# Kernel optimization log

Hardware: AMD Instinct MI355X
Metric: run time of the kernel (lower is better)

Reference implementation:

```python
import jax, jax.numpy as jnp
import numpy as np

B, L, D, H = 8192, 32, 128, 8  # batch nodes, max neighbors, embed dim, heads


def setup_inputs() -> dict:
    key = jax.random.key(0)
    ks = jax.random.split(key, 16)
    s = 0.05  # weight init scale
    return {
        "node_embeds": jax.random.normal(ks[0], (B, D), jnp.float32),
        "neighbor_embeds": jax.random.normal(ks[1], (B, L, D), jnp.float32),
        "node_degrees": jax.random.randint(ks[2], (B,), 1, L + 1),
        # layer 0 (concatenate=True): query_heads 128->1024, value_proj 128->128
        "wq0": jax.random.normal(ks[3], (H * D, D), jnp.float32) * s,
        "bq0": jax.random.normal(ks[4], (H * D,), jnp.float32) * s,
        "wv0": jax.random.normal(ks[5], (D, D), jnp.float32) * s,
        "bv0": jax.random.normal(ks[6], (D,), jnp.float32) * s,
        "wp0": jax.random.normal(ks[7], (D, D), jnp.float32) * s,
        "bp0": jax.random.normal(ks[8], (D,), jnp.float32) * s,
        # layer 1 (last, concatenate=False): query_heads 128->1024, value_proj 128->1024
        "wq1": jax.random.normal(ks[9], (H * D, D), jnp.float32) * s,
        "bq1": jax.random.normal(ks[10], (H * D,), jnp.float32) * s,
        "wv1": jax.random.normal(ks[11], (H * D, D), jnp.float32) * s,
        "bv1": jax.random.normal(ks[12], (H * D,), jnp.float32) * s,
        "wp1": jax.random.normal(ks[13], (D, D), jnp.float32) * s,
        "bp1": jax.random.normal(ks[14], (D,), jnp.float32) * s,
    }


def _attn_layer(node, neigh, mask, wq, bq, wv, bv, wp, bp, concatenate):
    # neigh: [B, L, D] (already zero-masked); mask: [B, L] bool
    b, l, d = neigh.shape
    dk = d  # attnhead_size == query_size == D for use_dot=True
    v = neigh @ wv.T + bv                      # [B, L, H*dv]
    dv = v.shape[-1] // H
    v = v.reshape(b, l, H, dv).transpose(0, 2, 1, 3)   # [B, H, L, dv]
    q = (node @ wq.T + bq).reshape(b, H, dk)           # [B, H, dk]
    scores = jnp.einsum('bhd,bld->bhl', q, neigh) / jnp.sqrt(jnp.float32(dk))
    scores = jnp.where(mask[:, None, :], scores, jnp.float32(-1e9))
    p = jax.nn.softmax(scores, axis=-1)                # [B, H, L]
    av = jnp.einsum('bhl,bhld->bhd', p, v)             # [B, H, dv]
    av = av.reshape(b, H * dv) if concatenate else av.mean(axis=1)
    return node @ wp.T + bp + av


def reference(node_embeds, neighbor_embeds, node_degrees,
              wq0, bq0, wv0, bv0, wp0, bp0,
              wq1, bq1, wv1, bv1, wp1, bp1):
    mask = jnp.arange(L)[None, :] < node_degrees[:, None]          # [B, L]
    neigh = jnp.where(mask[:, :, None], neighbor_embeds, 0.0)
    x = _attn_layer(node_embeds, neigh, mask, wq0, bq0, wv0, bv0, wp0, bp0, True)
    x = jax.nn.relu(x)  # activation on all but last layer
    x = _attn_layer(x, neigh, mask, wq1, bq1, wv1, bv1, wp1, bp1, False)
    return x
```

## Files before the change

kernel.cpp:

```cpp
#include <hip/hip_runtime.h>

constexpr int Ln = 32, Dn = 128, Hn = 8;

using bf16x8 = __attribute__((ext_vector_type(8))) short;
using f32x4  = __attribute__((ext_vector_type(4))) float;

__device__ __forceinline__ unsigned short f2bf(float f) {
    union { float f; unsigned u; } v; v.f = f;
    unsigned r = v.u + 0x7FFFu + ((v.u >> 16) & 1u);
    return (unsigned short)(r >> 16);
}
__device__ __forceinline__ float bf2f(unsigned short s) {
    union { unsigned u; float f; } v; v.u = ((unsigned)s) << 16; return v.f;
}
__device__ __forceinline__ bf16x8 cvt8(float4 a, float4 b) {
    bf16x8 r;
    r[0] = (short)f2bf(a.x); r[1] = (short)f2bf(a.y);
    r[2] = (short)f2bf(a.z); r[3] = (short)f2bf(a.w);
    r[4] = (short)f2bf(b.x); r[5] = (short)f2bf(b.y);
    r[6] = (short)f2bf(b.z); r[7] = (short)f2bf(b.w);
    return r;
}

constexpr int    CVT_ITEMS = 442368 + 2304;
constexpr size_t WS_NEED   = 442368ull * 2 + 2304ull * 4;

__global__ void cvt_weights(const float* __restrict__ wq0, const float* __restrict__ bq0,
                            const float* __restrict__ wv0, const float* __restrict__ bv0,
                            const float* __restrict__ wp0, const float* __restrict__ bp0,
                            const float* __restrict__ wq1, const float* __restrict__ bq1,
                            const float* __restrict__ wv1, const float* __restrict__ bv1,
                            const float* __restrict__ wp1, const float* __restrict__ bp1,
                            unsigned short* __restrict__ ws)
{
    const float scale = 0.08838834764831845f;
    int tid = blockIdx.x * 256 + threadIdx.x;
    if (tid >= CVT_ITEMS) return;
    if (tid < 442368) {
        float v;
        if      (tid < 131072) v = wq0[tid] * scale;
        else if (tid < 262144) v = wq1[tid - 131072] * scale;
        else if (tid < 278528) v = wv0[tid - 262144];
        else if (tid < 294912) v = wp0[tid - 278528];
        else if (tid < 425984) v = wv1[tid - 294912] * 0.125f;
        else                   v = wp1[tid - 425984];
        ws[tid] = f2bf(v);
    } else {
        int j = tid - 442368;
        float* fws = (float*)(ws + 442368);
        if      (j < 1024) fws[j] = bq0[j] * scale;
        else if (j < 2048) fws[j] = bq1[j - 1024] * scale;
        else if (j < 2176) { int d = j - 2048; fws[j] = bp0[d] + bv0[d]; }
        else if (j < 2304) {
            int d = j - 2176;
            float s = 0.f;
            #pragma unroll
            for (int h = 0; h < Hn; ++h) s += bv1[h * Dn + d];
            fws[j] = bp1[d] + 0.125f * s;
        }
    }
}

__global__ __launch_bounds__(512, 4)
void gcn15(const float* __restrict__ nodeE, const float* __restrict__ neighE,
           const int* __restrict__ degp, const unsigned short* __restrict__ ws,
           float* __restrict__ out)
{
    __shared__ unsigned short sN[8][16][136];
    __shared__ unsigned short sQC[16 * 1096];
    __shared__ unsigned short sX[16][136];
    __shared__ float          sP[8][16][Hn];
    __shared__ float          sSum[8][Hn];
    __shared__ int            sDeg[16];

    const unsigned short* wq0b = ws;
    const unsigned short* wq1b = ws + 131072;
    const unsigned short* wv0b = ws + 262144;
    const unsigned short* wp0b = ws + 278528;
    const unsigned short* wv1b = ws + 294912;
    const unsigned short* wp1b = ws + 425984;
    const float* fws  = (const float*)(ws + 442368);
    const float* bq0s = fws;
    const float* bq1s = fws + 1024;
    const float* b0   = fws + 2048;
    const float* b1   = fws + 2176;

    const int t    = threadIdx.x;
    const int lane = t & 63;
    const int w    = t >> 6;
    const int row  = lane & 15;
    const int kg   = lane >> 4;
    const int node0 = blockIdx.x * 16;

    bf16x8 a[4];

    auto stage_half = [&](int node, int r0, int v) {
        const float* base = neighE + ((size_t)(node0 + node) * Ln + r0) * Dn;
        #pragma unroll
        for (int it = 0; it < 4; ++it) {
            int c = lane + 64 * it;
            int l = c >> 4, d8 = c & 15;
            if (l < v) {
                const float4* s = (const float4*)(base + (size_t)c * 8);
                *(bf16x8*)&sN[w][l][d8 * 8] = cvt8(s[0], s[1]);
            }
        }
    };

    auto qgemm = [&](const unsigned short* wqb, const float* bqs) {
        #pragma unroll
        for (int ks = 0; ks < 4; ++ks)
            a[ks] = *(const bf16x8*)&sX[row][ks * 32 + kg * 8];
        #pragma unroll
        for (int f = 0; f < 8; ++f) {
            int o = w * 128 + f * 16 + row;
            f32x4 acc = {0.f, 0.f, 0.f, 0.f};
            #pragma unroll
            for (int ks = 0; ks < 4; ++ks)
                acc = __builtin_amdgcn_mfma_f32_16x16x32_bf16(
                    a[ks], *(const bf16x8*)(wqb + (size_t)o * Dn + ks * 32 + kg * 8), acc, 0, 0, 0);
            float bias = bqs[o];
            #pragma unroll
            for (int rr = 0; rr < 4; ++rr)
                sQC[(kg * 4 + rr) * 1096 + w * 136 + f * 16 + row] = f2bf(acc[rr] + bias);
        }
    };

    auto pv_acc = [&](float (&c)[Hn][2], int v) {
        #pragma unroll 2
        for (int l = 0; l < v; ++l) {
            unsigned nv = *(const unsigned*)&sN[w][l][2 * lane];
            float n0 = bf2f((unsigned short)(nv & 0xFFFFu));
            float n1 = bf2f((unsigned short)(nv >> 16));
            float4 p01 = *(const float4*)&sP[w][l][0];
            float4 p23 = *(const float4*)&sP[w][l][4];
            c[0][0] += p01.x * n0; c[0][1] += p01.x * n1;
            c[1][0] += p01.y * n0; c[1][1] += p01.y * n1;
            c[2][0] += p01.z * n0; c[2][1] += p01.z * n1;
            c[3][0] += p01.w * n0; c[3][1] += p01.w * n1;
            c[4][0] += p23.x * n0; c[4][1] += p23.x * n1;
            c[5][0] += p23.y * n0; c[5][1] += p23.y * n1;
            c[6][0] += p23.z * n0; c[6][1] += p23.z * n1;
            c[7][0] += p23.w * n0; c[7][1] += p23.w * n1;
        }
    };

    auto attn2 = [&](int node) {
        const int deg = sDeg[node];
        const int v0  = deg < 16 ? deg : 16;
        stage_half(node, 0, v0);

        const int hcol = row & 7;
        bf16x8 qf[4];
        #pragma unroll
        for (int ks = 0; ks < 4; ++ks)
            qf[ks] = *(const bf16x8*)&sQC[node * 1096 + hcol * 136 + ks * 32 + kg * 8];

        f32x4 s0 = {0.f,0.f,0.f,0.f};
        __builtin_amdgcn_s_setprio(1);
        #pragma unroll
        for (int ks = 0; ks < 4; ++ks)
            s0 = __builtin_amdgcn_mfma_f32_16x16x32_bf16(
                *(const bf16x8*)&sN[w][row][ks * 32 + kg * 8], qf[ks], s0, 0, 0, 0);
        __builtin_amdgcn_s_setprio(0);
        float sv[4];
        float sum = 0.f;
        #pragma unroll
        for (int j = 0; j < 4; ++j) {
            int l = kg * 4 + j;
            sv[j] = (l < v0) ? __expf(s0[j]) : 0.f;
            sum += sv[j];
        }
        sum += __shfl_xor(sum, 16);
        sum += __shfl_xor(sum, 32);
        if (row < 8) {
            #pragma unroll
            for (int j = 0; j < 4; ++j)
                sP[w][kg * 4 + j][row] = sv[j];
        }
        float c[Hn][2];
        #pragma unroll
        for (int h = 0; h < Hn; ++h) { c[h][0] = 0.f; c[h][1] = 0.f; }
        pv_acc(c, v0);

        if (deg > 16) {
            const int v1 = deg - 16;
            stage_half(node, 16, v1);
            f32x4 s1 = {0.f,0.f,0.f,0.f};
            __builtin_amdgcn_s_setprio(1);
            #pragma unroll
            for (int ks = 0; ks < 4; ++ks)
                s1 = __builtin_amdgcn_mfma_f32_16x16x32_bf16(
                    *(const bf16x8*)&sN[w][row][ks * 32 + kg * 8], qf[ks], s1, 0, 0, 0);
            __builtin_amdgcn_s_setprio(0);
            float sw[4];
            float sum1 = 0.f;
            #pragma unroll
            for (int j = 0; j < 4; ++j) {
                int l = kg * 4 + j;
                sw[j] = (l < v1) ? __expf(s1[j]) : 0.f;
                sum1 += sw[j];
            }
            sum1 += __shfl_xor(sum1, 16);
            sum1 += __shfl_xor(sum1, 32);
            sum += sum1;
            if (row < 8) {
                #pragma unroll
                for (int j = 0; j < 4; ++j)
                    sP[w][kg * 4 + j][row] = sw[j];
            }
            pv_acc(c, v1);
        }

        if (row < 8) sSum[w][row] = sum;
        float4 r01 = *(const float4*)&sSum[w][0];
        float4 r23 = *(const float4*)&sSum[w][4];
        float rh[Hn] = {r01.x, r01.y, r01.z, r01.w, r23.x, r23.y, r23.z, r23.w};
        #pragma unroll
        for (int h = 0; h < Hn; ++h) {
            float inv = 1.f / rh[h];
            unsigned pk = (unsigned)f2bf(c[h][0] * inv) | ((unsigned)f2bf(c[h][1] * inv) << 16);
            *(unsigned*)&sQC[node * 1096 + h * 136 + 2 * lane] = pk;
        }
    };

    if (t < 256) {
        int r = t >> 4, c = (t & 15) * 8;
        const float4* s = (const float4*)(nodeE + (size_t)(node0 + r) * Dn + c);
        *(bf16x8*)&sX[r][c] = cvt8(s[0], s[1]);
    }
    if (t < 16) sDeg[t] = degp[node0 + t];
    __syncthreads();

    qgemm(wq0b, bq0s);
    __syncthreads();

    attn2(w);
    attn2(8 + w);
    __syncthreads();

    {
        const int d = w * 16 + row;
        f32x4 pa = {0.f,0.f,0.f,0.f}, va = {0.f,0.f,0.f,0.f};
        #pragma unroll
        for (int ks = 0; ks < 4; ++ks) {
            pa = __builtin_amdgcn_mfma_f32_16x16x32_bf16(
                a[ks], *(const bf16x8*)(wp0b + (size_t)d * Dn + ks * 32 + kg * 8), pa, 0, 0, 0);
            bf16x8 c0 = *(const bf16x8*)&sQC[row * 1096 + w * 136 + ks * 32 + kg * 8];
            va = __builtin_amdgcn_mfma_f32_16x16x32_bf16(
                c0, *(const bf16x8*)(wv0b + (size_t)d * Dn + ks * 32 + kg * 8), va, 0, 0, 0);
        }
        float bias = b0[d];
        #pragma unroll
        for (int rr = 0; rr < 4; ++rr)
            sX[kg * 4 + rr][d] = f2bf(fmaxf(pa[rr] + va[rr] + bias, 0.f));
    }
    __syncthreads();

    qgemm(wq1b, bq1s);
    __syncthreads();

    attn2(w);
    attn2(8 + w);
    __syncthreads();

    {
        const int d = w * 16 + row;
        f32x4 pa = {0.f,0.f,0.f,0.f};
        #pragma unroll
        for (int ks = 0; ks < 4; ++ks)
            pa = __builtin_amdgcn_mfma_f32_16x16x32_bf16(
                a[ks], *(const bf16x8*)(wp1b + (size_t)d * Dn + ks * 32 + kg * 8), pa, 0, 0, 0);
        f32x4 g = {0.f,0.f,0.f,0.f};
        #pragma unroll 8
        for (int ks2 = 0; ks2 < 32; ++ks2) {
            int hk = ks2 * 32 + kg * 8;
            int h = hk >> 7, kk = hk & 127;
            bf16x8 c0 = *(const bf16x8*)&sQC[row * 1096 + h * 136 + kk];
            g = __builtin_amdgcn_mfma_f32_16x16x32_bf16(
                c0, *(const bf16x8*)(wv1b + ((size_t)(h * Dn + d)) * Dn + kk), g, 0, 0, 0);
        }
        float bias = b1[d];
        #pragma unroll
        for (int rr = 0; rr < 4; ++rr)
            out[(size_t)(node0 + kg * 4 + rr) * Dn + d] = pa[rr] + g[rr] + bias;
    }
}

__global__ __launch_bounds__(256, 2)
void gcn2(const float* __restrict__ nodeE, const float* __restrict__ neighE,
          const int* __restrict__ degp,
          const float* __restrict__ wq0, const float* __restrict__ bq0,
          const float* __restrict__ wv0, const float* __restrict__ bv0,
          const float* __restrict__ wp0, const float* __restrict__ bp0,
          const float* __restrict__ wq1, const float* __restrict__ bq1,
          const float* __restrict__ wv1, const float* __restrict__ bv1,
          const float* __restrict__ wp1, const float* __restrict__ bp1,
          float* __restrict__ out)
{
    __shared__ unsigned short sX[16][Dn];
    __shared__ unsigned short sQ[8][Hn][Dn];
    __shared__ unsigned short sN[4][Ln][Dn + 8];
    __shared__ float          sP[4][Hn][Ln];
    __shared__ unsigned short sC[8][Hn][Dn + 8];
    __shared__ int            sDeg[8];

    const int t    = threadIdx.x;
    const int lane = t & 63;
    const int w    = t >> 6;
    const int row  = lane & 15;
    const int kg   = lane >> 4;
    const int node0 = blockIdx.x * 8;
    const float scale = 0.08838834764831845f;

    {
        int i = t * 8, r = i >> 7, c = i & 127;
        if (r < 8) {
            const float4* s = (const float4*)(nodeE + (size_t)(node0 + r) * Dn + c);
            *(bf16x8*)&sX[r][c] = cvt8(s[0], s[1]);
        } else {
            bf16x8 z = {0,0,0,0,0,0,0,0};
            *(bf16x8*)&sX[r][c] = z;
        }
        if (t < 8) sDeg[t] = degp[node0 + t];
    }
    __syncthreads();

    auto qgemm = [&](const float* wq, const float* bq) {
        bf16x8 a[4];
        #pragma unroll
        for (int ks = 0; ks < 4; ++ks)
            a[ks] = *(const bf16x8*)&sX[row][ks*32 + kg*8];
        for (int f = 0; f < 16; ++f) {
            int o = w*256 + f*16 + row;
            f32x4 acc = {0.f, 0.f, 0.f, 0.f};
            #pragma unroll
            for (int ks = 0; ks < 4; ++ks) {
                const float4* wp4 = (const float4*)(wq + (size_t)o*Dn + ks*32 + kg*8);
                acc = __builtin_amdgcn_mfma_f32_16x16x32_bf16(a[ks], cvt8(wp4[0], wp4[1]), acc, 0, 0, 0);
            }
            float bias = bq[o];
            if (kg < 2) {
                #pragma unroll
                for (int rr = 0; rr < 4; ++rr) {
                    int nd = kg*4 + rr;
                    sQ[nd][o >> 7][o & 127] = f2bf((acc[rr] + bias) * scale);
                }
            }
        }
    };

    auto attn = [&](int b) {
        #pragma unroll
        for (int it = 0; it < 8; ++it) {
            int e8 = t + 256 * it;
            int n = e8 >> 9, l = (e8 >> 4) & 31, d8 = e8 & 15;
            const float4* s = (const float4*)(neighE + ((size_t)(node0 + b*4 + n)*Ln + l)*Dn + d8*8);
            *(bf16x8*)&sN[n][l][d8*8] = cvt8(s[0], s[1]);
        }
        __syncthreads();

        const int deg  = sDeg[b*4 + w];
        const int hcol = row & 7;
        bf16x8 qf[4];
        #pragma unroll
        for (int ks = 0; ks < 4; ++ks)
            qf[ks] = *(const bf16x8*)&sQ[b*4 + w][hcol][ks*32 + kg*8];

        f32x4 s0 = {0.f,0.f,0.f,0.f}, s1 = {0.f,0.f,0.f,0.f};
        #pragma unroll
        for (int ks = 0; ks < 4; ++ks) {
            bf16x8 a0 = *(const bf16x8*)&sN[w][row][ks*32 + kg*8];
            bf16x8 a1 = *(const bf16x8*)&sN[w][16 + row][ks*32 + kg*8];
            s0 = __builtin_amdgcn_mfma_f32_16x16x32_bf16(a0, qf[ks], s0, 0, 0, 0);
            s1 = __builtin_amdgcn_mfma_f32_16x16x32_bf16(a1, qf[ks], s1, 0, 0, 0);
        }
        float sv[8];
        #pragma unroll
        for (int rr = 0; rr < 4; ++rr) { sv[rr] = s0[rr]; sv[4+rr] = s1[rr]; }
        float m = -3.0e38f;
        #pragma unroll
        for (int j = 0; j < 8; ++j) {
            int l = (j >> 2)*16 + kg*4 + (j & 3);
            if (l >= deg) sv[j] = -3.0e38f;
            m = fmaxf(m, sv[j]);
        }
        m = fmaxf(m, __shfl_xor(m, 16));
        m = fmaxf(m, __shfl_xor(m, 32));
        float sum = 0.f;
        #pragma unroll
        for (int j = 0; j < 8; ++j) {
            float e = (sv[j] > -1.0e38f) ? __expf(sv[j] - m) : 0.f;
            sv[j] = e; sum += e;
        }
        sum += __shfl_xor(sum, 16);
        sum += __shfl_xor(sum, 32);
        float rinv = 1.f / sum;
        if (row < 8) {
            #pragma unroll
            for (int j = 0; j < 8; ++j) {
                int l = (j >> 2)*16 + kg*4 + (j & 3);
                sP[w][row][l] = sv[j] * rinv;
            }
        }

        float c[Hn][2];
        #pragma unroll
        for (int h = 0; h < Hn; ++h) { c[h][0] = 0.f; c[h][1] = 0.f; }
        #pragma unroll 4
        for (int l = 0; l < Ln; ++l) {
            unsigned nv = *(const unsigned*)&sN[w][l][2*lane];
            float n0 = bf2f((unsigned short)(nv & 0xFFFFu));
            float n1 = bf2f((unsigned short)(nv >> 16));
            #pragma unroll
            for (int h = 0; h < Hn; ++h) {
                float p = sP[w][h][l];
                c[h][0] += p * n0; c[h][1] += p * n1;
            }
        }
        #pragma unroll
        for (int h = 0; h < Hn; ++h) {
            unsigned pk = (unsigned)f2bf(c[h][0]) | ((unsigned)f2bf(c[h][1]) << 16);
            *(unsigned*)&sC[b*4 + w][h][2*lane] = pk;
        }
        __syncthreads();
    };

    auto ep0 = [&]() {
        bf16x8 a1[4];
        #pragma unroll
        for (int ks = 0; ks < 4; ++ks)
            a1[ks] = *(const bf16x8*)&sX[row][ks*32 + kg*8];
        float xn[2][4]; int dd[2];
        #pragma unroll
        for (int fi = 0; fi < 2; ++fi) {
            int f = 2*w + fi;
            int d = f*16 + row; dd[fi] = d;
            f32x4 acc = {0.f,0.f,0.f,0.f}, acc2 = {0.f,0.f,0.f,0.f};
            #pragma unroll
            for (int ks = 0; ks < 4; ++ks) {
                const float4* bp = (const float4*)(wp0 + (size_t)d*Dn + ks*32 + kg*8);
                acc = __builtin_amdgcn_mfma_f32_16x16x32_bf16(a1[ks], cvt8(bp[0], bp[1]), acc, 0, 0, 0);
                bf16x8 a2 = *(const bf16x8*)&sC[row & 7][f][ks*32 + kg*8];
                const float4* vp = (const float4*)(wv0 + (size_t)d*Dn + ks*32 + kg*8);
                acc2 = __builtin_amdgcn_mfma_f32_16x16x32_bf16(a2, cvt8(vp[0], vp[1]), acc2, 0, 0, 0);
            }
            float bias = bp0[d] + bv0[d];
            #pragma unroll
            for (int rr = 0; rr < 4; ++rr)
                xn[fi][rr] = fmaxf(acc[rr] + acc2[rr] + bias, 0.f);
        }
        __syncthreads();
        if (kg < 2) {
            #pragma unroll
            for (int fi = 0; fi < 2; ++fi)
                #pragma unroll
                for (int rr = 0; rr < 4; ++rr)
                    sX[kg*4 + rr][dd[fi]] = f2bf(xn[fi][rr]);
        }
        __syncthreads();
    };

    auto ep1 = [&]() {
        bf16x8 a1[4];
        #pragma unroll
        for (int ks = 0; ks < 4; ++ks)
            a1[ks] = *(const bf16x8*)&sX[row][ks*32 + kg*8];
        #pragma unroll
        for (int fi = 0; fi < 2; ++fi) {
            int f = 2*w + fi;
            int d = f*16 + row;
            f32x4 acc = {0.f,0.f,0.f,0.f};
            #pragma unroll
            for (int ks = 0; ks < 4; ++ks) {
                const float4* bp = (const float4*)(wp1 + (size_t)d*Dn + ks*32 + kg*8);
                acc = __builtin_amdgcn_mfma_f32_16x16x32_bf16(a1[ks], cvt8(bp[0], bp[1]), acc, 0, 0, 0);
            }
            f32x4 acc2 = {0.f,0.f,0.f,0.f};
            for (int ks2 = 0; ks2 < 32; ++ks2) {
                int hk = ks2*32 + kg*8;
                int h = hk >> 7, kk = hk & 127;
                bf16x8 a2 = *(const bf16x8*)&sC[row & 7][h][kk];
                const float4* vp = (const float4*)(wv1 + ((size_t)(h*Dn + d))*Dn + kk);
                acc2 = __builtin_amdgcn_mfma_f32_16x16x32_bf16(a2, cvt8(vp[0], vp[1]), acc2, 0, 0, 0);
            }
            float bsum = 0.f;
            #pragma unroll
            for (int h = 0; h < Hn; ++h) bsum += bv1[h*Dn + d];
            float bias = bp1[d] + 0.125f * bsum;
            if (kg < 2) {
                #pragma unroll
                for (int rr = 0; rr < 4; ++rr) {
                    int nd = kg*4 + rr;
                    out[(size_t)(node0 + nd)*Dn + d] = acc[rr] + 0.125f*acc2[rr] + bias;
                }
            }
        }
    };

    qgemm(wq0, bq0);
    __syncthreads();
    attn(0);
    attn(1);
    ep0();
    qgemm(wq1, bq1);
    __syncthreads();
    attn(0);
    attn(1);
    ep1();
}

extern "C" void kernel_launch(void* const* d_in, const int* in_sizes, int n_in,
                              void* d_out, int out_size, void* d_ws, size_t ws_size,
                              hipStream_t stream) {
    const float* nodeE  = (const float*)d_in[0];
    const float* neighE = (const float*)d_in[1];
    const int*   degp   = (const int*)d_in[2];
    const float* wq0 = (const float*)d_in[3];
    const float* bq0 = (const float*)d_in[4];
    const float* wv0 = (const float*)d_in[5];
    const float* bv0 = (const float*)d_in[6];
    const float* wp0 = (const float*)d_in[7];
    const float* bp0 = (const float*)d_in[8];
    const float* wq1 = (const float*)d_in[9];
    const float* bq1 = (const float*)d_in[10];
    const float* wv1 = (const float*)d_in[11];
    const float* bv1 = (const float*)d_in[12];
    const float* wp1 = (const float*)d_in[13];
    const float* bp1 = (const float*)d_in[14];
    float* outp = (float*)d_out;

    if (ws_size >= WS_NEED) {
        unsigned short* ws = (unsigned short*)d_ws;
        hipLaunchKernelGGL(cvt_weights, dim3((CVT_ITEMS + 255) / 256), dim3(256), 0, stream,
                           wq0, bq0, wv0, bv0, wp0, bp0,
                           wq1, bq1, wv1, bv1, wp1, bp1, ws);
        hipLaunchKernelGGL(gcn15, dim3(512), dim3(512), 0, stream,
                           nodeE, neighE, degp, ws, outp);
    } else {
        hipLaunchKernelGGL(gcn2, dim3(1024), dim3(256), 0, stream,
                           nodeE, neighE, degp,
                           wq0, bq0, wv0, bv0, wp0, bp0,
                           wq1, bq1, wv1, bv1, wp1, bp1, outp);
    }
}
```

Measured before the change: 83.36 us.

## Process eight nodes per 256-thread block with 8-neighbor attention chunks

Each block now handles 8 nodes with 4 waves instead of 16 nodes with 8 waves. The grid doubles to 1024 blocks, and the 16-row MFMA tiles are half padded with zero rows whose outputs are discarded. Attention now stages neighbors in chunks of 8 rows rather than 16, so low-degree nodes load and compute less. The aim is more blocks in flight and less wasted staging, paid for with MFMA work spent on padding rows and with each block re-reading the weights from cache for only half as many nodes.

```diff
diff --git a/kernel.cpp b/kernel.cpp
--- a/kernel.cpp
+++ b/kernel.cpp
@@ -61,17 +61,17 @@
     }
 }
 
-__global__ __launch_bounds__(512, 4)
-void gcn15(const float* __restrict__ nodeE, const float* __restrict__ neighE,
+__global__ __launch_bounds__(256, 5)
+void gcn16(const float* __restrict__ nodeE, const float* __restrict__ neighE,
            const int* __restrict__ degp, const unsigned short* __restrict__ ws,
            float* __restrict__ out)
 {
-    __shared__ unsigned short sN[8][16][136];
-    __shared__ unsigned short sQC[16 * 1096];
+    __shared__ unsigned short sN[4][8][136];
+    __shared__ unsigned short sQC[8 * 1096];
     __shared__ unsigned short sX[16][136];
-    __shared__ float          sP[8][16][Hn];
-    __shared__ float          sSum[8][Hn];
-    __shared__ int            sDeg[16];
+    __shared__ float          sP[4][8][Hn];
+    __shared__ float          sSum[4][Hn];
+    __shared__ int            sDeg[8];
 
     const unsigned short* wq0b = ws;
     const unsigned short* wq1b = ws + 131072;
@@ -90,14 +90,14 @@
     const int w    = t >> 6;
     const int row  = lane & 15;
     const int kg   = lane >> 4;
-    const int node0 = blockIdx.x * 16;
+    const int node0 = blockIdx.x * 8;
 
     bf16x8 a[4];
 
-    auto stage_half = [&](int node, int r0, int v) {
+    auto stage_q = [&](int node, int r0, int v) {
         const float* base = neighE + ((size_t)(node0 + node) * Ln + r0) * Dn;
         #pragma unroll
-        for (int it = 0; it < 4; ++it) {
+        for (int it = 0; it < 2; ++it) {
             int c = lane + 64 * it;
             int l = c >> 4, d8 = c & 15;
             if (l < v) {
@@ -112,17 +112,20 @@
         for (int ks = 0; ks < 4; ++ks)
             a[ks] = *(const bf16x8*)&sX[row][ks * 32 + kg * 8];
         #pragma unroll
-        for (int f = 0; f < 8; ++f) {
-            int o = w * 128 + f * 16 + row;
+        for (int f = 0; f < 16; ++f) {
+            int o = w * 256 + f * 16 + row;
             f32x4 acc = {0.f, 0.f, 0.f, 0.f};
             #pragma unroll
             for (int ks = 0; ks < 4; ++ks)
                 acc = __builtin_amdgcn_mfma_f32_16x16x32_bf16(
                     a[ks], *(const bf16x8*)(wqb + (size_t)o * Dn + ks * 32 + kg * 8), acc, 0, 0, 0);
             float bias = bqs[o];
-            #pragma unroll
-            for (int rr = 0; rr < 4; ++rr)
-                sQC[(kg * 4 + rr) * 1096 + w * 136 + f * 16 + row] = f2bf(acc[rr] + bias);
+            int h = o >> 7, d = o & 127;
+            if (kg < 2) {
+                #pragma unroll
+                for (int rr = 0; rr < 4; ++rr)
+                    sQC[(kg * 4 + rr) * 1096 + h * 136 + d] = f2bf(acc[rr] + bias);
+            }
         }
     };
 
@@ -145,71 +148,50 @@
         }
     };
 
-    auto attn2 = [&](int node) {
+    auto attn4 = [&](int node) {
         const int deg = sDeg[node];
-        const int v0  = deg < 16 ? deg : 16;
-        stage_half(node, 0, v0);
-
         const int hcol = row & 7;
         bf16x8 qf[4];
         #pragma unroll
         for (int ks = 0; ks < 4; ++ks)
             qf[ks] = *(const bf16x8*)&sQC[node * 1096 + hcol * 136 + ks * 32 + kg * 8];
 
-        f32x4 s0 = {0.f,0.f,0.f,0.f};
-        __builtin_amdgcn_s_setprio(1);
-        #pragma unroll
-        for (int ks = 0; ks < 4; ++ks)
-            s0 = __builtin_amdgcn_mfma_f32_16x16x32_bf16(
-                *(const bf16x8*)&sN[w][row][ks * 32 + kg * 8], qf[ks], s0, 0, 0, 0);
-        __builtin_amdgcn_s_setprio(0);
-        float sv[4];
         float sum = 0.f;
-        #pragma unroll
-        for (int j = 0; j < 4; ++j) {
-            int l = kg * 4 + j;
-            sv[j] = (l < v0) ? __expf(s0[j]) : 0.f;
-            sum += sv[j];
-        }
-        sum += __shfl_xor(sum, 16);
-        sum += __shfl_xor(sum, 32);
-        if (row < 8) {
-            #pragma unroll
-            for (int j = 0; j < 4; ++j)
-                sP[w][kg * 4 + j][row] = sv[j];
-        }
         float c[Hn][2];
         #pragma unroll
         for (int h = 0; h < Hn; ++h) { c[h][0] = 0.f; c[h][1] = 0.f; }
-        pv_acc(c, v0);
-
-        if (deg > 16) {
-            const int v1 = deg - 16;
-            stage_half(node, 16, v1);
-            f32x4 s1 = {0.f,0.f,0.f,0.f};
-            __builtin_amdgcn_s_setprio(1);
-            #pragma unroll
-            for (int ks = 0; ks < 4; ++ks)
-                s1 = __builtin_amdgcn_mfma_f32_16x16x32_bf16(
-                    *(const bf16x8*)&sN[w][row][ks * 32 + kg * 8], qf[ks], s1, 0, 0, 0);
-            __builtin_amdgcn_s_setprio(0);
-            float sw[4];
-            float sum1 = 0.f;
-            #pragma unroll
-            for (int j = 0; j < 4; ++j) {
-                int l = kg * 4 + j;
-                sw[j] = (l < v1) ? __expf(s1[j]) : 0.f;
-                sum1 += sw[j];
-            }
-            sum1 += __shfl_xor(sum1, 16);
-            sum1 += __shfl_xor(sum1, 32);
-            sum += sum1;
-            if (row < 8) {
-                #pragma unroll
-                for (int j = 0; j < 4; ++j)
-                    sP[w][kg * 4 + j][row] = sw[j];
-            }
-            pv_acc(c, v1);
+
+        #pragma unroll
+        for (int tt = 0; tt < 4; ++tt) {
+            int r0 = tt * 8;
+            if (r0 < deg) {
+                int v = deg - r0; v = v < 8 ? v : 8;
+                stage_q(node, r0, v);
+                f32x4 s0 = {0.f,0.f,0.f,0.f};
+                __builtin_amdgcn_s_setprio(1);
+                #pragma unroll
+                for (int ks = 0; ks < 4; ++ks)
+                    s0 = __builtin_amdgcn_mfma_f32_16x16x32_bf16(
+                        *(const bf16x8*)&sN[w][row][ks * 32 + kg * 8], qf[ks], s0, 0, 0, 0);
+                __builtin_amdgcn_s_setprio(0);
+                float sv[4];
+                float ps = 0.f;
+                #pragma unroll
+                for (int j = 0; j < 4; ++j) {
+                    int l = kg * 4 + j;
+                    sv[j] = (l < v) ? __expf(s0[j]) : 0.f;
+                    ps += sv[j];
+                }
+                ps += __shfl_xor(ps, 16);
+                ps += __shfl_xor(ps, 32);
+                sum += ps;
+                if (row < 8 && kg < 2) {
+                    #pragma unroll
+                    for (int j = 0; j < 4; ++j)
+                        sP[w][kg * 4 + j][row] = sv[j];
+                }
+                pv_acc(c, v);
+            }
         }
 
         if (row < 8) sSum[w][row] = sum;
@@ -224,66 +206,93 @@
         }
     };
 
-    if (t < 256) {
+    {
         int r = t >> 4, c = (t & 15) * 8;
-        const float4* s = (const float4*)(nodeE + (size_t)(node0 + r) * Dn + c);
-        *(bf16x8*)&sX[r][c] = cvt8(s[0], s[1]);
+        bf16x8 v;
+        if (r < 8) {
+            const float4* s = (const float4*)(nodeE + (size_t)(node0 + r) * Dn + c);
+            v = cvt8(s[0], s[1]);
+        } else {
+            bf16x8 z = {0,0,0,0,0,0,0,0}; v = z;
+        }
+        *(bf16x8*)&sX[r][c] = v;
     }
-    if (t < 16) sDeg[t] = degp[node0 + t];
+    if (t < 8) sDeg[t] = degp[node0 + t];
     __syncthreads();
 
     qgemm(wq0b, bq0s);
     __syncthreads();
 
-    attn2(w);
-    attn2(8 + w);
+    attn4(w);
+    attn4(4 + w);
     __syncthreads();
 
     {
-        const int d = w * 16 + row;
-        f32x4 pa = {0.f,0.f,0.f,0.f}, va = {0.f,0.f,0.f,0.f};
+        float xn[2][4]; int dd[2];
+        #pragma unroll
+        for (int fi = 0; fi < 2; ++fi) {
+            const int h = 2 * w + fi;
+            const int d = h * 16 + row; dd[fi] = d;
+            f32x4 pa = {0.f,0.f,0.f,0.f}, va = {0.f,0.f,0.f,0.f};
+            #pragma unroll
+            for (int ks = 0; ks < 4; ++ks) {
+                pa = __builtin_amdgcn_mfma_f32_16x16x32_bf16(
+                    a[ks], *(const bf16x8*)(wp0b + (size_t)d * Dn + ks * 32 + kg * 8), pa, 0, 0, 0);
+                bf16x8 c0 = *(const bf16x8*)&sQC[row * 1096 + h * 136 + ks * 32 + kg * 8];
+                va = __builtin_amdgcn_mfma_f32_16x16x32_bf16(
+                    c0, *(const bf16x8*)(wv0b + (size_t)d * Dn + ks * 32 + kg * 8), va, 0, 0, 0);
+            }
+            float bias = b0[d];
+            #pragma unroll
+            for (int rr = 0; rr < 4; ++rr)
+                xn[fi][rr] = fmaxf(pa[rr] + va[rr] + bias, 0.f);
+        }
+        if (kg < 2) {
+            #pragma unroll
+            for (int fi = 0; fi < 2; ++fi)
+                #pragma unroll
+                for (int rr = 0; rr < 4; ++rr)
+                    sX[kg * 4 + rr][dd[fi]] = f2bf(xn[fi][rr]);
+        }
+    }
+    __syncthreads();
+
+    qgemm(wq1b, bq1s);
+    __syncthreads();
+
+    attn4(w);
+    attn4(4 + w);
+    __syncthreads();
+
+    {
+        const int d0 = w * 32 + row;
+        const int d1 = d0 + 16;
+        f32x4 p0 = {0.f,0.f,0.f,0.f}, p1 = {0.f,0.f,0.f,0.f};
         #pragma unroll
         for (int ks = 0; ks < 4; ++ks) {
-            pa = __builtin_amdgcn_mfma_f32_16x16x32_bf16(
-                a[ks], *(const bf16x8*)(wp0b + (size_t)d * Dn + ks * 32 + kg * 8), pa, 0, 0, 0);
-            bf16x8 c0 = *(const bf16x8*)&sQC[row * 1096 + w * 136 + ks * 32 + kg * 8];
-            va = __builtin_amdgcn_mfma_f32_16x16x32_bf16(
-                c0, *(const bf16x8*)(wv0b + (size_t)d * Dn + ks * 32 + kg * 8), va, 0, 0, 0);
-        }
-        float bias = b0[d];
-        #pragma unroll
-        for (int rr = 0; rr < 4; ++rr)
-            sX[kg * 4 + rr][d] = f2bf(fmaxf(pa[rr] + va[rr] + bias, 0.f));
-    }
-    __syncthreads();
-
-    qgemm(wq1b, bq1s);
-    __syncthreads();
-
-    attn2(w);
-    attn2(8 + w);
-    __syncthreads();
-
-    {
-        const int d = w * 16 + row;
-        f32x4 pa = {0.f,0.f,0.f,0.f};
-        #pragma unroll
-        for (int ks = 0; ks < 4; ++ks)
-            pa = __builtin_amdgcn_mfma_f32_16x16x32_bf16(
-                a[ks], *(const bf16x8*)(wp1b + (size_t)d * Dn + ks * 32 + kg * 8), pa, 0, 0, 0);
-        f32x4 g = {0.f,0.f,0.f,0.f};
+            p0 = __builtin_amdgcn_mfma_f32_16x16x32_bf16(
+                a[ks], *(const bf16x8*)(wp1b + (size_t)d0 * Dn + ks * 32 + kg * 8), p0, 0, 0, 0);
+            p1 = __builtin_amdgcn_mfma_f32_16x16x32_bf16(
+                a[ks], *(const bf16x8*)(wp1b + (size_t)d1 * Dn + ks * 32 + kg * 8), p1, 0, 0, 0);
+        }
+        f32x4 g0 = {0.f,0.f,0.f,0.f}, g1 = {0.f,0.f,0.f,0.f};
         #pragma unroll 8
         for (int ks2 = 0; ks2 < 32; ++ks2) {
             int hk = ks2 * 32 + kg * 8;
             int h = hk >> 7, kk = hk & 127;
             bf16x8 c0 = *(const bf16x8*)&sQC[row * 1096 + h * 136 + kk];
-            g = __builtin_amdgcn_mfma_f32_16x16x32_bf16(
-                c0, *(const bf16x8*)(wv1b + ((size_t)(h * Dn + d)) * Dn + kk), g, 0, 0, 0);
-        }
-        float bias = b1[d];
-        #pragma unroll
-        for (int rr = 0; rr < 4; ++rr)
-            out[(size_t)(node0 + kg * 4 + rr) * Dn + d] = pa[rr] + g[rr] + bias;
+            g0 = __builtin_amdgcn_mfma_f32_16x16x32_bf16(
+                c0, *(const bf16x8*)(wv1b + ((size_t)(h * Dn + d0)) * Dn + kk), g0, 0, 0, 0);
+            g1 = __builtin_amdgcn_mfma_f32_16x16x32_bf16(
+                c0, *(const bf16x8*)(wv1b + ((size_t)(h * Dn + d1)) * Dn + kk), g1, 0, 0, 0);
+        }
+        if (kg < 2) {
+            #pragma unroll
+            for (int rr = 0; rr < 4; ++rr) {
+                out[(size_t)(node0 + kg * 4 + rr) * Dn + d0] = p0[rr] + g0[rr] + b1[d0];
+                out[(size_t)(node0 + kg * 4 + rr) * Dn + d1] = p1[rr] + g1[rr] + b1[d1];
+            }
+        }
     }
 }
 
@@ -535,7 +544,7 @@
         hipLaunchKernelGGL(cvt_weights, dim3((CVT_ITEMS + 255) / 256), dim3(256), 0, stream,
                            wq0, bq0, wv0, bv0, wp0, bp0,
                            wq1, bq1, wv1, bv1, wp1, bp1, ws);
-        hipLaunchKernelGGL(gcn15, dim3(512), dim3(512), 0, stream,
+        hipLaunchKernelGGL(gcn16, dim3(1024), dim3(256), 0, stream,
                            nodeE, neighE, degp, ws, outp);
     } else {
         hipLaunchKernelGGL(gcn2, dim3(1024), dim3(256), 0, stream,
```

Result: slower. 156.0 us (+87.2%).
